# Performance work log

Hardware: AMD Instinct MI355X
Metric: run time of the kernel (lower is better)

The kernel has to match this reference:

```python
import jax, jax.numpy as jnp
import numpy as np

HID = 512


def _lstm_cell(x, h, c, W_ih, W_hh, b):
    # torch gate order: i, f, g, o ; z: [B, 4H]
    z = x @ W_ih.T + h @ W_hh.T + b
    i, f, g, o = jnp.split(z, 4, axis=-1)
    c_new = jax.nn.sigmoid(f) * c + jax.nn.sigmoid(i) * jnp.tanh(g)
    h_new = jax.nn.sigmoid(o) * jnp.tanh(c_new)
    return h_new, c_new


def setup_inputs() -> dict:
    key = jax.random.key(0)
    ks = jax.random.split(key, 10)
    s = 1.0 / np.sqrt(HID)  # torch default LSTM init scale
    return {
        "inputs": jax.random.normal(ks[0], (512, 512, 1), jnp.float32),
        "targets": jax.random.normal(ks[1], (512, 128, 1), jnp.float32),
        "enc_Wih": jax.random.uniform(ks[2], (4 * HID, 1), jnp.float32, -s, s),
        "enc_Whh": jax.random.uniform(ks[3], (4 * HID, HID), jnp.float32, -s, s),
        "enc_b": jax.random.uniform(ks[4], (4 * HID,), jnp.float32, -s, s),
        "dec_Wih": jax.random.uniform(ks[5], (4 * HID, 1), jnp.float32, -s, s),
        "dec_Whh": jax.random.uniform(ks[6], (4 * HID, HID), jnp.float32, -s, s),
        "dec_b": jax.random.uniform(ks[7], (4 * HID,), jnp.float32, -s, s),
        "lin_W": jax.random.uniform(ks[8], (1, HID), jnp.float32, -s, s),
        "lin_b": jax.random.uniform(ks[9], (1,), jnp.float32, -s, s),
        "target_len": 128,
        "teacher_forcing_ratio": 0,
    }


def reference(inputs, targets, enc_Wih, enc_Whh, enc_b,
              dec_Wih, dec_Whh, dec_b, lin_W, lin_b,
              target_len, teacher_forcing_ratio):
    B = inputs.shape[0]
    H = enc_Whh.shape[1]
    h0 = jnp.zeros((B, H), inputs.dtype)
    c0 = jnp.zeros((B, H), inputs.dtype)

    # ---- encoder: scan over source timesteps ----
    def enc_step(carry, x_t):  # x_t: [B, 1]
        h, c = carry
        h, c = _lstm_cell(x_t, h, c, enc_Wih, enc_Whh, enc_b)
        return (h, c), None

    (h, c), _ = jax.lax.scan(enc_step, (h0, c0), jnp.swapaxes(inputs, 0, 1))

    x0 = inputs[:, -1, :]  # [B, 1]

    def dec_step(carry, _):
        h, c, x = carry
        h, c = _lstm_cell(x, h, c, dec_Wih, dec_Whh, dec_b)
        out = h @ lin_W.T + lin_b  # [B, 1]
        return (h, c, out), out

    _, outs = jax.lax.scan(dec_step, (h, c, x0), None, length=target_len)
    return jnp.swapaxes(outs, 0, 1)  # [B, target_len, 1]
```

## Files before the change

### kernel.cpp

```cpp
#include <hip/hip_runtime.h>
#include <math.h>

#define HID    512
#define BATCH  512
#define TIN    512
#define TOUT   128
#define FOUR_H 2048
#define STEPS  (TIN + TOUT)

typedef __bf16 bf16x8 __attribute__((ext_vector_type(8)));
typedef float floatx4 __attribute__((ext_vector_type(4)));
typedef int   int4v   __attribute__((ext_vector_type(4)));

#define GLOADX4_SC(dst, p) \
    asm volatile("global_load_dwordx4 %0, %1, off sc0 sc1" : "=v"(dst) : "v"(p))
#define GSTOREX4_SC(p, v) \
    asm volatile("global_store_dwordx4 %0, %1, off sc0 sc1" :: "v"(p), "v"(v) : "memory")
#define GLOADX4_C(dst, p) \
    asm volatile("global_load_dwordx4 %0, %1, off" : "=v"(dst) : "v"(p))
#define WAIT_T1(N, r) asm volatile("s_waitcnt vmcnt(" #N ")" : "+v"(r))
#define WAIT_T4(N, B) asm volatile("s_waitcnt vmcnt(" #N ")" \
    : "+v"((B)[0]), "+v"((B)[1]), "+v"((B)[2]), "+v"((B)[3]))

__device__ __forceinline__ float fsig(float x) {
    return __builtin_amdgcn_rcpf(1.0f + __expf(-x));
}
__device__ __forceinline__ float ftanh(float x) {
    return 1.0f - 2.0f * __builtin_amdgcn_rcpf(1.0f + __expf(2.0f * x));
}

__global__ __launch_bounds__(256) void pack_w(
    const float* __restrict__ W, __bf16* __restrict__ Apk)
{
    int tid = blockIdx.x * 256 + threadIdx.x;
    int mp  = tid >> 6;
    int kg  = tid & 63;
    int g   = mp & 3;
    int j   = mp >> 2;
    int r   = g * HID + j;
    int blk   = mp >> 7;
    int rg    = (mp >> 4) & 7;
    int lr    = mp & 15;
    int chunk = kg >> 2;
    int lq    = kg & 3;
    int lane  = lq * 16 + lr;
    const float* src = W + (size_t)r * HID + kg * 8;
    size_t offHi = ((size_t)(((blk * 8 + rg) * 16 + chunk) * 2 + 0) * 512) + lane * 8;
    size_t offLo = ((size_t)(((blk * 8 + rg) * 16 + chunk) * 2 + 1) * 512) + lane * 8;
    __bf16 hibuf[8], lobuf[8];
    #pragma unroll
    for (int i = 0; i < 8; ++i) {
        float x = src[i];
        __bf16 hi = (__bf16)x;
        hibuf[i] = hi;
        lobuf[i] = (__bf16)(x - (float)hi);
    }
    *(bf16x8*)(Apk + offHi) = *(bf16x8*)hibuf;
    *(bf16x8*)(Apk + offLo) = *(bf16x8*)lobuf;
}

__global__ __launch_bounds__(256) void pack_v(
    const float* __restrict__ Wih, const float* __restrict__ b,
    float* __restrict__ WihP, float* __restrict__ bP)
{
    int mp = blockIdx.x * 256 + threadIdx.x;
    int g  = mp & 3;
    int j  = mp >> 2;
    int r  = g * HID + j;
    WihP[mp] = Wih[r];
    bP[mp]   = b[r];
}

__global__ __launch_bounds__(256) void transpose_in(
    const float* __restrict__ in, float* __restrict__ outT)
{
    int idx = blockIdx.x * 256 + threadIdx.x;
    int t = idx >> 9, b = idx & 511;
    outT[idx] = in[(size_t)b * TIN + t];
}

__global__ __launch_bounds__(256, 1) void lstm_persistent(
    const __bf16* __restrict__ ApkEnc,
    const __bf16* __restrict__ ApkDec,
    const float* __restrict__ WihPenc, const float* __restrict__ biasPenc,
    const float* __restrict__ WihPdec, const float* __restrict__ biasPdec,
    const float* __restrict__ inputsT,
    const float* __restrict__ linW, const float* __restrict__ linb,
    __bf16* __restrict__ h0,
    __bf16* __restrict__ h1,
    float* __restrict__ xacc,
    int* __restrict__ barrier_ws,
    float* __restrict__ out)
{
    extern __shared__ char smem[];
    __bf16* Alds   = (__bf16*)smem;
    char*   Bring  = smem + 131072;
    __bf16* hstage = (__bf16*)(smem + 147456);
    float*  xred   = (float*)(smem + 151552);

    const int tid  = threadIdx.x;
    const int lane = tid & 63;
    const int w    = tid >> 6;
    const int lr   = lane & 15;
    const int lq   = lane >> 4;
    const int by   = blockIdx.x >> 4;
    const int blk  = blockIdx.x & 15;
    const int nbase = by * 32;
    const int rgbase = 2 * w;
    const bool STREAM = (w >= 2);

    const int m0a = blk * 128 + (rgbase + 0) * 16 + lq * 4;
    const int m0b = blk * 128 + (rgbase + 1) * 16 + lq * 4;
    const floatx4 wihE[2] = { *(const floatx4*)(WihPenc + m0a), *(const floatx4*)(WihPenc + m0b) };
    const floatx4 bE[2]   = { *(const floatx4*)(biasPenc + m0a), *(const floatx4*)(biasPenc + m0b) };
    const floatx4 wihD[2] = { *(const floatx4*)(WihPdec + m0a), *(const floatx4*)(WihPdec + m0b) };
    const floatx4 bD[2]   = { *(const floatx4*)(biasPdec + m0a), *(const floatx4*)(biasPdec + m0b) };
    const float lw[2] = { linW[m0a >> 2], linW[m0b >> 2] };
    const float lb = linb[0];

    int bn[2];
    #pragma unroll
    for (int nt = 0; nt < 2; ++nt) bn[nt] = nbase + nt * 16 + lr;

    {
        const int4v* srcp = (const int4v*)(ApkEnc + (size_t)blk * 131072);
        int4v* dstp = (int4v*)Alds;
        for (int i = tid; i < 8192; i += 256) dstp[i] = srcp[i];
    }
    __syncthreads();

    float creg[2][2] = {{0.f, 0.f}, {0.f, 0.f}};

    int* arrive = barrier_ws + by * 32;
    int* phase  = barrier_ws + 512 + by * 32;

    for (int s = 0; s < STEPS; ++s) {
        const bool dec = (s >= TIN);
        const int  t   = s - TIN;
        const __bf16* Acur = dec ? ApkDec : ApkEnc;

        if (s == TIN) {
            const int4v* srcp = (const int4v*)(ApkDec + (size_t)blk * 131072);
            int4v* dstp = (int4v*)Alds;
            for (int i = tid; i < 8192; i += 256) dstp[i] = srcp[i];
            __syncthreads();
        }

        const __bf16* hin  = (s & 1) ? h1 : h0;
        __bf16*       hout = (s & 1) ? h0 : h1;
        const __bf16* srcB = hin + (size_t)by * 32768 + tid * 8;
        const __bf16* Ag   = Acur + (size_t)blk * 131072;

        float xq[2];
        if (dec) {
            if (tid < 32) xred[tid] = 0.f;
            if (blk == 0) {
                if (t >= 1 && tid < 32) {
                    float v = __hip_atomic_load(&xacc[((t - 1) % 3) * BATCH + nbase + tid],
                                                __ATOMIC_RELAXED, __HIP_MEMORY_SCOPE_AGENT) + lb;
                    out[(size_t)(nbase + tid) * TOUT + (t - 1)] = v;
                }
                if (tid >= 32 && tid < 64) {
                    __hip_atomic_store(&xacc[((t + 1) % 3) * BATCH + nbase + (tid - 32)], 0.0f,
                                       __ATOMIC_RELAXED, __HIP_MEMORY_SCOPE_AGENT);
                }
            }
            #pragma unroll
            for (int nt = 0; nt < 2; ++nt)
                xq[nt] = (t == 0) ? inputsT[(TIN - 1) * BATCH + bn[nt]]
                                  : __hip_atomic_load(&xacc[((t - 1) % 3) * BATCH + bn[nt]],
                                                      __ATOMIC_RELAXED, __HIP_MEMORY_SCOPE_AGENT) + lb;
        } else {
            #pragma unroll
            for (int nt = 0; nt < 2; ++nt)
                xq[nt] = inputsT[s * BATCH + bn[nt]];
        }
        asm volatile("" ::: "memory");

        int4v st[4];
        int4v areg[2][4];
        GLOADX4_SC(st[0], srcB + 0 * 2048);
        GLOADX4_SC(st[1], srcB + 1 * 2048);
        if (STREAM) {
            #pragma unroll
            for (int mb = 0; mb < 2; ++mb)
                #pragma unroll
                for (int pl = 0; pl < 2; ++pl)
                    GLOADX4_C(areg[0][mb * 2 + pl],
                              Ag + (size_t)((((rgbase + mb) * 16 + 0) * 2 + pl) * 512) + lane * 8);
        }
        GLOADX4_SC(st[2], srcB + 2 * 2048);

        floatx4 acc[2][2];
        #pragma unroll
        for (int mb = 0; mb < 2; ++mb)
            #pragma unroll
            for (int nt = 0; nt < 2; ++nt) acc[mb][nt] = floatx4{0.f, 0.f, 0.f, 0.f};

        #pragma unroll
        for (int it = 0; it < 16; ++it) {
            if (STREAM) {
                if      (it <= 13) { WAIT_T1(6, st[it & 3]); }
                else if (it == 14) { WAIT_T1(5, st[it & 3]); }
                else               { WAIT_T1(4, st[it & 3]); }
            } else {
                if      (it <= 13) { WAIT_T1(2, st[it & 3]); }
                else if (it == 14) { WAIT_T1(1, st[it & 3]); }
                else               { WAIT_T1(0, st[it & 3]); }
            }
            *(int4v*)(Bring + (it & 3) * 4096 + tid * 16) = st[it & 3];

            if (STREAM && it + 1 < 16) {
                #pragma unroll
                for (int mb = 0; mb < 2; ++mb)
                    #pragma unroll
                    for (int pl = 0; pl < 2; ++pl)
                        GLOADX4_C(areg[(it + 1) & 1][mb * 2 + pl],
                                  Ag + (size_t)((((rgbase + mb) * 16 + (it + 1)) * 2 + pl) * 512) + lane * 8);
            }
            if (it + 3 < 16) GLOADX4_SC(st[(it + 3) & 3], srcB + (it + 3) * 2048);

            __syncthreads();

            bf16x8 ah[2], al[2];
            if (STREAM) {
                if      (it <= 12) { WAIT_T4(6, areg[it & 1]); }
                else if (it == 13) { WAIT_T4(5, areg[it & 1]); }
                else if (it == 14) { WAIT_T4(4, areg[it & 1]); }
                else               { WAIT_T4(0, areg[it & 1]); }
                #pragma unroll
                for (int mb = 0; mb < 2; ++mb) {
                    ah[mb] = __builtin_bit_cast(bf16x8, areg[it & 1][mb * 2 + 0]);
                    al[mb] = __builtin_bit_cast(bf16x8, areg[it & 1][mb * 2 + 1]);
                }
            } else {
                #pragma unroll
                for (int mb = 0; mb < 2; ++mb) {
                    const char* ap = (const char*)Alds
                        + (((rgbase + mb) * 16 + it) * 2) * 1024 + lane * 16;
                    ah[mb] = *(const bf16x8*)(ap);
                    al[mb] = *(const bf16x8*)(ap + 1024);
                }
            }

            const char* bs = Bring + (it & 3) * 4096;
            bf16x8 bh0 = *(const bf16x8*)(bs + (0 * 128 + 0 * 64 + lane) * 16);
            bf16x8 bl0 = *(const bf16x8*)(bs + (0 * 128 + 1 * 64 + lane) * 16);
            bf16x8 bh1 = *(const bf16x8*)(bs + (1 * 128 + 0 * 64 + lane) * 16);
            bf16x8 bl1 = *(const bf16x8*)(bs + (1 * 128 + 1 * 64 + lane) * 16);

            #pragma unroll
            for (int mb = 0; mb < 2; ++mb) {
                acc[mb][0] = __builtin_amdgcn_mfma_f32_16x16x32_bf16(ah[mb], bh0, acc[mb][0], 0, 0, 0);
                acc[mb][1] = __builtin_amdgcn_mfma_f32_16x16x32_bf16(ah[mb], bh1, acc[mb][1], 0, 0, 0);
                acc[mb][0] = __builtin_amdgcn_mfma_f32_16x16x32_bf16(al[mb], bh0, acc[mb][0], 0, 0, 0);
                acc[mb][1] = __builtin_amdgcn_mfma_f32_16x16x32_bf16(al[mb], bh1, acc[mb][1], 0, 0, 0);
                acc[mb][0] = __builtin_amdgcn_mfma_f32_16x16x32_bf16(ah[mb], bl0, acc[mb][0], 0, 0, 0);
                acc[mb][1] = __builtin_amdgcn_mfma_f32_16x16x32_bf16(ah[mb], bl1, acc[mb][1], 0, 0, 0);
            }
        }

        const floatx4* wih = dec ? wihD : wihE;
        const floatx4* bb  = dec ? bD   : bE;
        float px[2] = {0.f, 0.f};
        #pragma unroll
        for (int mb = 0; mb < 2; ++mb) {
            const int jlocal = (rgbase + mb) * 4 + lq;
            #pragma unroll
            for (int nt = 0; nt < 2; ++nt) {
                float x  = xq[nt];
                float i_ = fsig (acc[mb][nt][0] + bb[mb][0] + x * wih[mb][0]);
                float f_ = fsig (acc[mb][nt][1] + bb[mb][1] + x * wih[mb][1]);
                float g_ = ftanh(acc[mb][nt][2] + bb[mb][2] + x * wih[mb][2]);
                float o_ = fsig (acc[mb][nt][3] + bb[mb][3] + x * wih[mb][3]);
                float cv = f_ * creg[mb][nt] + i_ * g_;
                creg[mb][nt] = cv;
                float h  = o_ * ftanh(cv);
                __bf16 hh = (__bf16)h;
                int bl = nt * 16 + lr;
                hstage[bl * 32 + jlocal] = hh;
                hstage[1024 + bl * 32 + jlocal] = (__bf16)(h - (float)hh);
                if (dec) {
                    float v = h * lw[mb];
                    px[nt] += v;
                }
            }
        }
        if (dec) {
            #pragma unroll
            for (int nt = 0; nt < 2; ++nt) {
                px[nt] += __shfl_xor(px[nt], 16);
                px[nt] += __shfl_xor(px[nt], 32);
            }
        }

        __syncthreads();

        {
            int nt = tid >> 7, pl = (tid >> 6) & 1, ln = tid & 63;
            int kq = ln >> 4, lrp = ln & 15;
            const char* src = (const char*)hstage + pl * 2048 + (nt * 16 + lrp) * 64 + kq * 16;
            int4v v = *(const int4v*)src;
            __bf16* dst = hout + (size_t)by * 32768 + blk * 2048 + tid * 8;
            GSTOREX4_SC(dst, v);
        }

        if (dec && lane < 16) {
            #pragma unroll
            for (int nt = 0; nt < 2; ++nt) atomicAdd(&xred[nt * 16 + lr], px[nt]);
        }
        __syncthreads();
        if (dec && tid < 32) {
            atomicAdd(&xacc[(t % 3) * BATCH + nbase + tid], xred[tid]);
        }

        __builtin_amdgcn_s_waitcnt(0);
        __syncthreads();
        if (tid == 0) {
            int n = __hip_atomic_fetch_add(arrive, 1, __ATOMIC_RELAXED, __HIP_MEMORY_SCOPE_AGENT);
            if (n == 16 * (s + 1) - 1) {
                __hip_atomic_store(phase, s + 1, __ATOMIC_RELAXED, __HIP_MEMORY_SCOPE_AGENT);
            } else {
                int p;
                do {
                    __builtin_amdgcn_s_sleep(2);
                    p = __hip_atomic_load(phase, __ATOMIC_RELAXED, __HIP_MEMORY_SCOPE_AGENT);
                } while (p < s + 1);
            }
        }
        __syncthreads();
    }

    if (blk == 0 && tid < 32) {
        float v = __hip_atomic_load(&xacc[((TOUT - 1) % 3) * BATCH + nbase + tid],
                                    __ATOMIC_RELAXED, __HIP_MEMORY_SCOPE_AGENT) + lb;
        out[(size_t)(nbase + tid) * TOUT + (TOUT - 1)] = v;
    }
}

extern "C" void kernel_launch(void* const* d_in, const int* in_sizes, int n_in,
                              void* d_out, int out_size, void* d_ws, size_t ws_size,
                              hipStream_t stream) {
    const float* inputs  = (const float*)d_in[0];
    const float* enc_Wih = (const float*)d_in[2];
    const float* enc_Whh = (const float*)d_in[3];
    const float* enc_b   = (const float*)d_in[4];
    const float* dec_Wih = (const float*)d_in[5];
    const float* dec_Whh = (const float*)d_in[6];
    const float* dec_b   = (const float*)d_in[7];
    const float* lin_W   = (const float*)d_in[8];
    const float* lin_b   = (const float*)d_in[9];
    float* out = (float*)d_out;

    char* ws = (char*)d_ws;
    const size_t SZ_APK = (size_t)FOUR_H * HID * 2 * sizeof(__bf16);
    const size_t SZ_V   = (size_t)FOUR_H * sizeof(float);
    const size_t SZ_HF  = (size_t)16 * 16 * 256 * 8 * sizeof(__bf16);

    __bf16* ApkEnc = (__bf16*)(ws);
    __bf16* ApkDec = (__bf16*)(ws + SZ_APK);
    char* p = ws + 2 * SZ_APK;
    float* WihPenc  = (float*)p;  p += SZ_V;
    float* biasPenc = (float*)p;  p += SZ_V;
    float* WihPdec  = (float*)p;  p += SZ_V;
    float* biasPdec = (float*)p;  p += SZ_V;
    float* inputsT  = (float*)p;  p += (size_t)TIN * BATCH * sizeof(float);
    __bf16* h0 = (__bf16*)p;      p += SZ_HF;
    __bf16* h1 = (__bf16*)p;      p += SZ_HF;
    float* xacc  = (float*)p;     p += 3 * BATCH * sizeof(float);
    int* barrier_ws = (int*)p;    p += 1024 * sizeof(int);

    pack_w<<<512, 256, 0, stream>>>(enc_Whh, ApkEnc);
    pack_w<<<512, 256, 0, stream>>>(dec_Whh, ApkDec);
    pack_v<<<8, 256, 0, stream>>>(enc_Wih, enc_b, WihPenc, biasPenc);
    pack_v<<<8, 256, 0, stream>>>(dec_Wih, dec_b, WihPdec, biasPdec);
    transpose_in<<<1024, 256, 0, stream>>>(inputs, inputsT);
    hipMemsetAsync(h0, 0, SZ_HF, stream);
    hipMemsetAsync(xacc, 0, 3 * BATCH * sizeof(float), stream);
    hipMemsetAsync(barrier_ws, 0, 1024 * sizeof(int), stream);

    const int shmem = 131072 + 16384 + 4096 + 128;
    hipFuncSetAttribute((const void*)lstm_persistent,
                        hipFuncAttributeMaxDynamicSharedMemorySize, shmem);

    void* args[] = {
        (void*)&ApkEnc, (void*)&ApkDec,
        (void*)&WihPenc, (void*)&biasPenc, (void*)&WihPdec, (void*)&biasPdec,
        (void*)&inputsT, (void*)&lin_W, (void*)&lin_b,
        (void*)&h0, (void*)&h1,
        (void*)&xacc, (void*)&barrier_ws, (void*)&out
    };
    hipLaunchCooperativeKernel((void*)lstm_persistent, dim3(256), dim3(256),
                               args, shmem, stream);
}
```

Baseline: 4.434 ms.

## Rotate K-chunk order per block and consume own h chunk from LDS staging

Each block now walks the 16 K-chunks of h starting at its own index, so its first chunk is the h slice it just computed, read directly from the local LDS staging buffer instead of from global memory. This drops one global load and one block barrier per step and staggers which global chunks different blocks fetch first, spreading contention. The staging buffer is padded to a 40-element row stride, intended to cut LDS bank conflicts, and is zeroed at start for step zero. The cost is more complex wait counts and a small increase in LDS use.

```diff
diff --git a/kernel.cpp b/kernel.cpp
--- a/kernel.cpp
+++ b/kernel.cpp
@@ -96,7 +96,7 @@
     __bf16* Alds   = (__bf16*)smem;
     char*   Bring  = smem + 131072;
     __bf16* hstage = (__bf16*)(smem + 147456);
-    float*  xred   = (float*)(smem + 151552);
+    float*  xred   = (float*)(smem + 152576);
 
     const int tid  = threadIdx.x;
     const int lane = tid & 63;
@@ -123,6 +123,10 @@
     for (int nt = 0; nt < 2; ++nt) bn[nt] = nbase + nt * 16 + lr;
 
     {
+        float* hz = (float*)hstage;
+        for (int i = tid; i < 1280; i += 256) hz[i] = 0.f;
+    }
+    {
         const int4v* srcp = (const int4v*)(ApkEnc + (size_t)blk * 131072);
         int4v* dstp = (int4v*)Alds;
         for (int i = tid; i < 8192; i += 256) dstp[i] = srcp[i];
@@ -179,17 +183,16 @@
 
         int4v st[4];
         int4v areg[2][4];
-        GLOADX4_SC(st[0], srcB + 0 * 2048);
-        GLOADX4_SC(st[1], srcB + 1 * 2048);
+        GLOADX4_SC(st[1], srcB + (size_t)((blk + 1) & 15) * 2048);
+        GLOADX4_SC(st[2], srcB + (size_t)((blk + 2) & 15) * 2048);
         if (STREAM) {
             #pragma unroll
             for (int mb = 0; mb < 2; ++mb)
                 #pragma unroll
                 for (int pl = 0; pl < 2; ++pl)
                     GLOADX4_C(areg[0][mb * 2 + pl],
-                              Ag + (size_t)((((rgbase + mb) * 16 + 0) * 2 + pl) * 512) + lane * 8);
-        }
-        GLOADX4_SC(st[2], srcB + 2 * 2048);
+                              Ag + (size_t)((((rgbase + mb) * 16 + blk) * 2 + pl) * 512) + lane * 8);
+        }
 
         floatx4 acc[2][2];
         #pragma unroll
@@ -199,35 +202,42 @@
 
         #pragma unroll
         for (int it = 0; it < 16; ++it) {
-            if (STREAM) {
-                if      (it <= 13) { WAIT_T1(6, st[it & 3]); }
-                else if (it == 14) { WAIT_T1(5, st[it & 3]); }
-                else               { WAIT_T1(4, st[it & 3]); }
-            } else {
-                if      (it <= 13) { WAIT_T1(2, st[it & 3]); }
-                else if (it == 14) { WAIT_T1(1, st[it & 3]); }
-                else               { WAIT_T1(0, st[it & 3]); }
-            }
-            *(int4v*)(Bring + (it & 3) * 4096 + tid * 16) = st[it & 3];
+            const int c = (blk + it) & 15;
+
+            if (it > 0) {
+                if (STREAM) {
+                    if      (it == 1 || it == 14) { WAIT_T1(5, st[it & 3]); }
+                    else if (it <= 13)            { WAIT_T1(6, st[it & 3]); }
+                    else                          { WAIT_T1(4, st[it & 3]); }
+                } else {
+                    if      (it <= 13) { WAIT_T1(2, st[it & 3]); }
+                    else if (it == 14) { WAIT_T1(1, st[it & 3]); }
+                    else               { WAIT_T1(0, st[it & 3]); }
+                }
+                *(int4v*)(Bring + (it & 3) * 4096 + tid * 16) = st[it & 3];
+            }
 
             if (STREAM && it + 1 < 16) {
+                const int cn = (blk + it + 1) & 15;
                 #pragma unroll
                 for (int mb = 0; mb < 2; ++mb)
                     #pragma unroll
                     for (int pl = 0; pl < 2; ++pl)
                         GLOADX4_C(areg[(it + 1) & 1][mb * 2 + pl],
-                                  Ag + (size_t)((((rgbase + mb) * 16 + (it + 1)) * 2 + pl) * 512) + lane * 8);
-            }
-            if (it + 3 < 16) GLOADX4_SC(st[(it + 3) & 3], srcB + (it + 3) * 2048);
-
-            __syncthreads();
+                                  Ag + (size_t)((((rgbase + mb) * 16 + cn) * 2 + pl) * 512) + lane * 8);
+            }
+            if (it + 3 < 16)
+                GLOADX4_SC(st[(it + 3) & 3], srcB + (size_t)((blk + it + 3) & 15) * 2048);
+
+            if (it > 0) __syncthreads();
 
             bf16x8 ah[2], al[2];
             if (STREAM) {
-                if      (it <= 12) { WAIT_T4(6, areg[it & 1]); }
-                else if (it == 13) { WAIT_T4(5, areg[it & 1]); }
-                else if (it == 14) { WAIT_T4(4, areg[it & 1]); }
-                else               { WAIT_T4(0, areg[it & 1]); }
+                if      (it == 0)  { WAIT_T4(5, areg[0]); }
+                else if (it <= 12) { WAIT_T4(6, areg[it & 1]); }
+                else if (it == 13) { WAIT_T4(5, areg[1]); }
+                else if (it == 14) { WAIT_T4(4, areg[0]); }
+                else               { WAIT_T4(0, areg[1]); }
                 #pragma unroll
                 for (int mb = 0; mb < 2; ++mb) {
                     ah[mb] = __builtin_bit_cast(bf16x8, areg[it & 1][mb * 2 + 0]);
@@ -237,17 +247,27 @@
                 #pragma unroll
                 for (int mb = 0; mb < 2; ++mb) {
                     const char* ap = (const char*)Alds
-                        + (((rgbase + mb) * 16 + it) * 2) * 1024 + lane * 16;
+                        + (((rgbase + mb) * 16 + c) * 2) * 1024 + lane * 16;
                     ah[mb] = *(const bf16x8*)(ap);
                     al[mb] = *(const bf16x8*)(ap + 1024);
                 }
             }
 
-            const char* bs = Bring + (it & 3) * 4096;
-            bf16x8 bh0 = *(const bf16x8*)(bs + (0 * 128 + 0 * 64 + lane) * 16);
-            bf16x8 bl0 = *(const bf16x8*)(bs + (0 * 128 + 1 * 64 + lane) * 16);
-            bf16x8 bh1 = *(const bf16x8*)(bs + (1 * 128 + 0 * 64 + lane) * 16);
-            bf16x8 bl1 = *(const bf16x8*)(bs + (1 * 128 + 1 * 64 + lane) * 16);
+            bf16x8 bh0, bl0, bh1, bl1;
+            if (it == 0) {
+                const char* hb = (const char*)hstage;
+                const int kq = lane >> 4, lrp = lane & 15;
+                bh0 = *(const bf16x8*)(hb + (     lrp) * 80 + kq * 16);
+                bl0 = *(const bf16x8*)(hb + (32 + lrp) * 80 + kq * 16);
+                bh1 = *(const bf16x8*)(hb + (16 + lrp) * 80 + kq * 16);
+                bl1 = *(const bf16x8*)(hb + (48 + lrp) * 80 + kq * 16);
+            } else {
+                const char* bs = Bring + (it & 3) * 4096;
+                bh0 = *(const bf16x8*)(bs + (0 * 128 + 0 * 64 + lane) * 16);
+                bl0 = *(const bf16x8*)(bs + (0 * 128 + 1 * 64 + lane) * 16);
+                bh1 = *(const bf16x8*)(bs + (1 * 128 + 0 * 64 + lane) * 16);
+                bl1 = *(const bf16x8*)(bs + (1 * 128 + 1 * 64 + lane) * 16);
+            }
 
             #pragma unroll
             for (int mb = 0; mb < 2; ++mb) {
@@ -278,8 +298,8 @@
                 float h  = o_ * ftanh(cv);
                 __bf16 hh = (__bf16)h;
                 int bl = nt * 16 + lr;
-                hstage[bl * 32 + jlocal] = hh;
-                hstage[1024 + bl * 32 + jlocal] = (__bf16)(h - (float)hh);
+                hstage[bl * 40 + jlocal] = hh;
+                hstage[(32 + bl) * 40 + jlocal] = (__bf16)(h - (float)hh);
                 if (dec) {
                     float v = h * lw[mb];
                     px[nt] += v;
@@ -299,7 +319,7 @@
         {
             int nt = tid >> 7, pl = (tid >> 6) & 1, ln = tid & 63;
             int kq = ln >> 4, lrp = ln & 15;
-            const char* src = (const char*)hstage + pl * 2048 + (nt * 16 + lrp) * 64 + kq * 16;
+            const char* src = (const char*)hstage + (pl * 32 + nt * 16 + lrp) * 80 + kq * 16;
             int4v v = *(const int4v*)src;
             __bf16* dst = hout + (size_t)by * 32768 + blk * 2048 + tid * 8;
             GSTOREX4_SC(dst, v);
@@ -379,7 +399,7 @@
     hipMemsetAsync(xacc, 0, 3 * BATCH * sizeof(float), stream);
     hipMemsetAsync(barrier_ws, 0, 1024 * sizeof(int), stream);
 
-    const int shmem = 131072 + 16384 + 4096 + 128;
+    const int shmem = 131072 + 16384 + 5120 + 128;
     hipFuncSetAttribute((const void*)lstm_persistent,
                         hipFuncAttributeMaxDynamicSharedMemorySize, shmem);
 
```

After: 4.426 ms. No clear change (-0.2%).
